# Kernel optimization log

Hardware: AMD Instinct MI355X
Metric: run time of the kernel (lower is better)

## Reference

```python
import jax, jax.numpy as jnp
import numpy as np

D_MODEL = 1024
H = 16
D_K = D_MODEL // H
D_FF = 4096
EPS = 1e-6


def setup_inputs() -> dict:
    key = jax.random.key(0)
    ks = jax.random.split(key, 16)
    s = 1.0 / np.sqrt(D_MODEL)
    sf = 1.0 / np.sqrt(D_FF)
    inp = {
        'x': jax.random.normal(ks[0], (4, 2048, D_MODEL), dtype=jnp.float32),
        'wq': jax.random.uniform(ks[1], (D_MODEL, D_MODEL), minval=-s, maxval=s),
        'bq': jax.random.uniform(ks[2], (D_MODEL,), minval=-s, maxval=s),
        'wk': jax.random.uniform(ks[3], (D_MODEL, D_MODEL), minval=-s, maxval=s),
        'bk': jax.random.uniform(ks[4], (D_MODEL,), minval=-s, maxval=s),
        'wv': jax.random.uniform(ks[5], (D_MODEL, D_MODEL), minval=-s, maxval=s),
        'bv': jax.random.uniform(ks[6], (D_MODEL,), minval=-s, maxval=s),
        'wo': jax.random.uniform(ks[7], (D_MODEL, D_MODEL), minval=-s, maxval=s),
        'bo': jax.random.uniform(ks[8], (D_MODEL,), minval=-s, maxval=s),
        'w1': jax.random.uniform(ks[9], (D_MODEL, D_FF), minval=-s, maxval=s),
        'b1': jax.random.uniform(ks[10], (D_FF,), minval=-s, maxval=s),
        'w2': jax.random.uniform(ks[11], (D_FF, D_MODEL), minval=-sf, maxval=sf),
        'b2': jax.random.uniform(ks[12], (D_MODEL,), minval=-sf, maxval=sf),
        'alpha1': jnp.ones((1,), jnp.float32),
        'bias1': jnp.zeros((1,), jnp.float32),
        'alpha2': jnp.ones((1,), jnp.float32),
        'bias2': jnp.zeros((1,), jnp.float32),
    }
    return inp


def _layer_norm(x, alpha, bias):
    # torch: alpha*(x-mean)/(std+eps)+bias with unbiased std (ddof=1), eps on std
    m = jnp.mean(x, axis=-1, keepdims=True)
    s = jnp.std(x, axis=-1, keepdims=True, ddof=1)
    return alpha * (x - m) / (s + EPS) + bias


def _mha(x, wq, bq, wk, bk, wv, bv, wo, bo):
    B, S, _ = x.shape
    q = (x @ wq + bq).reshape(B, S, H, D_K).transpose(0, 2, 1, 3)
    k = (x @ wk + bk).reshape(B, S, H, D_K).transpose(0, 2, 1, 3)
    v = (x @ wv + bv).reshape(B, S, H, D_K).transpose(0, 2, 1, 3)
    scores = jnp.einsum('bhqd,bhkd->bhqk', q, k) / np.sqrt(D_K)
    attn = jax.nn.softmax(scores, axis=-1)
    out = jnp.einsum('bhqk,bhkd->bhqd', attn, v)
    out = out.transpose(0, 2, 1, 3).reshape(B, S, D_MODEL)
    return out @ wo + bo


def reference(x, wq, bq, wk, bk, wv, bv, wo, bo, w1, b1, w2, b2,
              alpha1, bias1, alpha2, bias2):
    # Residual 1: x + MHA(LN(x))
    h = x + _mha(_layer_norm(x, alpha1, bias1), wq, bq, wk, bk, wv, bv, wo, bo)
    # Residual 2: h + FFN(LN(h)); FFN = W2 relu(W1 z + b1) + b2
    z = _layer_norm(h, alpha2, bias2)
    ffn = jax.nn.relu(z @ w1 + b1) @ w2 + b2
    return h + ffn
```

## Files before the change

### kernel.cpp

```cpp
#include <hip/hip_runtime.h>
#include <hip/hip_bf16.h>
#include <cstdint>
#include <cstddef>

typedef __bf16 bf16;
typedef __bf16 bf16x4 __attribute__((ext_vector_type(4)));
typedef __bf16 bf16x8 __attribute__((ext_vector_type(8)));
typedef float f32x4 __attribute__((ext_vector_type(4)));

#define AS1 __attribute__((address_space(1)))
#define AS3 __attribute__((address_space(3)))

__device__ __forceinline__ void gload_lds16(const void* g, void* l) {
  __builtin_amdgcn_global_load_lds((AS1 void*)g, (AS3 void*)l, 16, 0, 0);
}

__global__ __launch_bounds__(256)
void transpose_cvt(const float* __restrict__ in, bf16* __restrict__ out,
                   int K, int N) {
  __shared__ float t[32][33];
  const int tx = threadIdx.x, ty = threadIdx.y;
  const int n0 = blockIdx.x * 32, k0 = blockIdx.y * 32;
#pragma unroll
  for (int j = ty; j < 32; j += 8)
    t[j][tx] = in[(size_t)(k0 + j) * N + n0 + tx];
  __syncthreads();
#pragma unroll
  for (int j = ty; j < 32; j += 8)
    out[(size_t)(n0 + j) * K + k0 + tx] = (bf16)t[tx][j];
}

__global__ __launch_bounds__(256)
void concat_bias(const float* __restrict__ bq, const float* __restrict__ bk,
                 const float* __restrict__ bv, float* __restrict__ o) {
  int i = blockIdx.x * 256 + threadIdx.x;
  if (i < 1024) o[i] = bq[i];
  else if (i < 2048) o[i] = bk[i - 1024];
  else o[i] = bv[i - 2048];
}

__global__ __launch_bounds__(256)
void ln_kernel(const float* __restrict__ x, bf16* __restrict__ y,
               const float* __restrict__ alpha_p, const float* __restrict__ beta_p) {
  const int row = blockIdx.x;
  const float4 v = ((const float4*)(x + (size_t)row * 1024))[threadIdx.x];
  float s = v.x + v.y + v.z + v.w;
  float ss = v.x * v.x + v.y * v.y + v.z * v.z + v.w * v.w;
#pragma unroll
  for (int m = 1; m < 64; m <<= 1) {
    s += __shfl_xor(s, m);
    ss += __shfl_xor(ss, m);
  }
  __shared__ float red[8];
  const int wave = threadIdx.x >> 6, lane = threadIdx.x & 63;
  if (lane == 0) { red[wave] = s; red[4 + wave] = ss; }
  __syncthreads();
  s = red[0] + red[1] + red[2] + red[3];
  ss = red[4] + red[5] + red[6] + red[7];
  const float mean = s * (1.0f / 1024.0f);
  const float var = fmaxf(ss - 1024.0f * mean * mean, 0.0f) * (1.0f / 1023.0f);
  const float k = alpha_p[0] / (sqrtf(var) + 1e-6f);
  const float beta = beta_p[0];
  union { bf16 b[4]; uint2 u; } pk;
  pk.b[0] = (bf16)((v.x - mean) * k + beta);
  pk.b[1] = (bf16)((v.y - mean) * k + beta);
  pk.b[2] = (bf16)((v.z - mean) * k + beta);
  pk.b[3] = (bf16)((v.w - mean) * k + beta);
  ((uint2*)(y + (size_t)row * 1024))[threadIdx.x] = pk.u;
}

template <typename OutT, bool RELU, bool RESID>
__global__ __launch_bounds__(256)
void gemm_bt(const bf16* __restrict__ A, const bf16* __restrict__ Bt,
             const float* __restrict__ bias, const float* __restrict__ resid,
             OutT* __restrict__ C, int M, int N, int K) {
  __shared__ __align__(16) bf16 As[2][128 * 32];
  __shared__ __align__(16) bf16 Bs[2][128 * 32];
  const int tid = threadIdx.x;
  const int wave = tid >> 6, lane = tid & 63;
  const int l16 = lane & 15, lq = lane >> 4;
  const int nwg = gridDim.x * gridDim.y;
  const int id = blockIdx.y * gridDim.x + blockIdx.x;
  const int w = (id & 7) * (nwg >> 3) + (id >> 3);
  const int bm = (w / gridDim.y) * 128, bn = (w % gridDim.y) * 128;
  const int wr = wave >> 1, wc = wave & 1;

  const int tmp = (lane * 16) ^ (((lane >> 3) & 7) << 4);
  const int srow = tmp >> 6, sseg = (tmp >> 4) & 3;
  const bf16* Ab = A + (size_t)bm * K + sseg * 8;
  const bf16* Bb = Bt + (size_t)bn * K + sseg * 8;

  auto STAGE = [&](int k0, int buf) {
#pragma unroll
    for (int i = 0; i < 2; i++) {
      const int chunk = wave * 2 + i;
      const int r = chunk * 16 + srow;
      gload_lds16(Ab + (size_t)r * K + k0, (char*)As[buf] + chunk * 1024);
      gload_lds16(Bb + (size_t)r * K + k0, (char*)Bs[buf] + chunk * 1024);
    }
  };
  auto swz = [&](int row) -> int {
    return (row >> 1) * 128 + (((((row & 1) << 2) | lq) ^ ((row >> 1) & 7)) << 4);
  };

  STAGE(0, 0);
  __syncthreads();

  f32x4 acc[4][4] = {};
  const int nk = K >> 5;
  for (int t = 0; t < nk; t++) {
    const int cur = t & 1;
    if (t + 1 < nk) STAGE((t + 1) << 5, cur ^ 1);
    bf16x8 a[4], b[4];
#pragma unroll
    for (int m = 0; m < 4; m++)
      a[m] = *(const bf16x8*)((const char*)As[cur] + swz(wr * 64 + m * 16 + l16));
#pragma unroll
    for (int n = 0; n < 4; n++)
      b[n] = *(const bf16x8*)((const char*)Bs[cur] + swz(wc * 64 + n * 16 + l16));
#pragma unroll
    for (int m = 0; m < 4; m++)
#pragma unroll
      for (int n = 0; n < 4; n++)
        acc[m][n] = __builtin_amdgcn_mfma_f32_16x16x32_bf16(a[m], b[n], acc[m][n], 0, 0, 0);
    __syncthreads();
  }
#pragma unroll
  for (int m = 0; m < 4; m++) {
    const int row0 = bm + wr * 64 + m * 16 + lq * 4;
#pragma unroll
    for (int n = 0; n < 4; n++) {
      const int col = bn + wc * 64 + n * 16 + l16;
      const float bv = bias[col];
#pragma unroll
      for (int j = 0; j < 4; j++) {
        float v = acc[m][n][j] + bv;
        if (RELU) v = fmaxf(v, 0.0f);
        if (RESID) v += resid[(size_t)(row0 + j) * N + col];
        C[(size_t)(row0 + j) * N + col] = (OutT)v;
      }
    }
  }
}

__global__ __launch_bounds__(256)
void vt_prep(const bf16* __restrict__ qkv, bf16* __restrict__ Vt) {
  __shared__ __align__(16) bf16 Vl[64 * 64];
  const int tid = threadIdx.x;
  const int sblk = blockIdx.x, bh = blockIdx.y, b = bh >> 4, h = bh & 15;
  const size_t srow = (size_t)b * 2048 + sblk * 64;
  const bf16* src = qkv + srow * 3072 + 2048 + h * 64;
#pragma unroll
  for (int i = 0; i < 2; i++) {
    int c = i * 256 + tid;
    int s = c >> 3, dseg = c & 7;
    int col = dseg ^ (s & 7) ^ (s >> 3);
    *(uint4*)((char*)Vl + s * 128 + col * 16) =
        *(const uint4*)(src + (size_t)s * 3072 + dseg * 8);
  }
  __syncthreads();
  bf16* dst = Vt + (size_t)bh * 64 * 2048 + sblk * 64;
#pragma unroll
  for (int i = 0; i < 2; i++) {
    int c = i * 256 + tid;
    int d = c >> 3, grp = c & 7;
    union { bf16 v[8]; uint4 u; } pk;
#pragma unroll
    for (int j = 0; j < 8; j++) {
      int s = grp * 8 + j;
      int col = (d >> 3) ^ (s & 7) ^ (s >> 3);
      pk.v[j] = *(const bf16*)((char*)Vl + s * 128 + col * 16 + ((2 * d) & 15));
    }
    *(uint4*)(dst + (size_t)d * 2048 + grp * 8) = pk.u;
  }
}

__global__ __launch_bounds__(256, 2)
void attn_kernel(const bf16* __restrict__ qkv, const bf16* __restrict__ Vt,
                 bf16* __restrict__ out) {
  __shared__ __align__(16) bf16 smem[32768];
  bf16* Qs = smem;
  bf16* Ks = smem + 16384;
  bf16* Vs = smem + 24576;
  const int tid = threadIdx.x, wave = tid >> 6, lane = tid & 63;
  const int l16 = lane & 15, lq = lane >> 4;
  const int id = blockIdx.y * 8 + blockIdx.x;
  const int w = (id & 7) * 64 + (id >> 3);
  const int qblk = w & 7, bh = w >> 3;
  const int b = bh >> 4, h = bh & 15;
  const int q0 = qblk * 256;
  const size_t rowbase = (size_t)b * 2048;
  const bf16* Qg = qkv + (rowbase + q0) * 3072 + h * 64;
  const bf16* Kg = qkv + rowbase * 3072 + 1024 + h * 64;
  const bf16* Vg = Vt + (size_t)bh * 64 * 2048;

#pragma unroll
  for (int i = 0; i < 8; i++) {
    const int c = i * 256 + wave * 64;
    const int cl = c + lane;
    const int r = cl >> 3, seg = cl & 7;
    gload_lds16(Qg + (size_t)r * 3072 + (seg ^ (r & 7)) * 8, (char*)Qs + c * 16);
  }
  auto stageKV = [&](int kt, int buf) {
    const int kv0 = kt * 64;
#pragma unroll
    for (int i = 0; i < 2; i++) {
      const int c = i * 256 + wave * 64;
      const int cl = c + lane;
      const int r = cl >> 3, seg = cl & 7;
      gload_lds16(Kg + (size_t)(kv0 + r) * 3072 + (seg ^ (r & 7)) * 8,
                  (char*)Ks + buf * 8192 + c * 16);
      gload_lds16(Vg + (size_t)r * 2048 + kv0 + (seg ^ (r & 7)) * 8,
                  (char*)Vs + buf * 8192 + c * 16);
    }
  };
  stageKV(0, 0);

  f32x4 oacc[4][4] = {};
  f32x4 lacc[4] = {};
  bf16x8 qb[4][2];
  bf16x8 onesb;
#pragma unroll
  for (int j = 0; j < 8; j++) onesb[j] = (bf16)1.0f;

  for (int t = 0; t < 32; t++) {
    const int cur = t & 1;
    __builtin_amdgcn_s_barrier();
    if (t < 31) stageKV(t + 1, cur ^ 1);
    if (t < 31) asm volatile("s_waitcnt vmcnt(4)" ::: "memory");
    else        asm volatile("s_waitcnt vmcnt(0)" ::: "memory");
    __builtin_amdgcn_s_barrier();
    const char* Kb = (const char*)Ks + cur * 8192;
    const char* Vb = (const char*)Vs + cur * 8192;

    if (t == 0) {
#pragma unroll
      for (int g = 0; g < 4; g++)
#pragma unroll
        for (int H = 0; H < 2; H++) {
          const int row = wave * 64 + g * 16 + l16;
          const int col = (H * 64 + lq * 16) ^ ((row & 7) << 4);
          qb[g][H] = *(const bf16x8*)((const char*)Qs + row * 128 + col);
        }
    }
    bf16x8 ka[2][4];
#pragma unroll
    for (int H = 0; H < 2; H++)
#pragma unroll
      for (int m = 0; m < 4; m++) {
        const int row = m * 16 + l16;
        const int col = (H * 64 + lq * 16) ^ ((row & 7) << 4);
        ka[H][m] = *(const bf16x8*)(Kb + row * 128 + col);
      }
    bf16x8 vb[2][4];
#pragma unroll
    for (int H = 0; H < 2; H++)
#pragma unroll
      for (int nd = 0; nd < 4; nd++) {
        const int row = nd * 16 + l16;
        const int xorv = (row & 7) << 4;
        const int c1 = (H * 64 + lq * 8) ^ xorv;
        const int c2 = (H * 64 + lq * 8 + 32) ^ xorv;
        bf16x4 lo = *(const bf16x4*)(Vb + row * 128 + c1);
        bf16x4 hi = *(const bf16x4*)(Vb + row * 128 + c2);
        vb[H][nd] = __builtin_shufflevector(lo, hi, 0, 1, 2, 3, 4, 5, 6, 7);
      }
#pragma unroll
    for (int g = 0; g < 4; g++) {
      f32x4 sc[4];
#pragma unroll
      for (int m = 0; m < 4; m++) {
        f32x4 z = {};
        sc[m] = __builtin_amdgcn_mfma_f32_16x16x32_bf16(ka[0][m], qb[g][0], z, 0, 0, 0);
        sc[m] = __builtin_amdgcn_mfma_f32_16x16x32_bf16(ka[1][m], qb[g][1], sc[m], 0, 0, 0);
      }
      bf16x8 pa0, pa1;
#pragma unroll
      for (int m = 0; m < 2; m++)
#pragma unroll
        for (int r = 0; r < 4; r++)
          pa0[m * 4 + r] = (bf16)__builtin_amdgcn_exp2f(sc[m][r] * 0.1803368801f);
#pragma unroll
      for (int m = 0; m < 2; m++)
#pragma unroll
        for (int r = 0; r < 4; r++)
          pa1[m * 4 + r] = (bf16)__builtin_amdgcn_exp2f(sc[2 + m][r] * 0.1803368801f);
#pragma unroll
      for (int nd = 0; nd < 4; nd++) {
        oacc[g][nd] = __builtin_amdgcn_mfma_f32_16x16x32_bf16(pa0, vb[0][nd], oacc[g][nd], 0, 0, 0);
        oacc[g][nd] = __builtin_amdgcn_mfma_f32_16x16x32_bf16(pa1, vb[1][nd], oacc[g][nd], 0, 0, 0);
      }
      lacc[g] = __builtin_amdgcn_mfma_f32_16x16x32_bf16(pa0, onesb, lacc[g], 0, 0, 0);
      lacc[g] = __builtin_amdgcn_mfma_f32_16x16x32_bf16(pa1, onesb, lacc[g], 0, 0, 0);
    }
  }
#pragma unroll
  for (int g = 0; g < 4; g++) {
#pragma unroll
    for (int r = 0; r < 4; r++) {
      const float inv = 1.0f / lacc[g][r];
      const size_t row = rowbase + q0 + wave * 64 + g * 16 + lq * 4 + r;
#pragma unroll
      for (int nd = 0; nd < 4; nd++)
        out[row * 1024 + h * 64 + nd * 16 + l16] = (bf16)(oacc[g][nd][r] * inv);
    }
  }
}

extern "C" void kernel_launch(void* const* d_in, const int* in_sizes, int n_in,
                              void* d_out, int out_size, void* d_ws, size_t ws_size,
                              hipStream_t stream) {
  const float* x      = (const float*)d_in[0];
  const float* wq     = (const float*)d_in[1];
  const float* bq     = (const float*)d_in[2];
  const float* wk     = (const float*)d_in[3];
  const float* bk     = (const float*)d_in[4];
  const float* wv     = (const float*)d_in[5];
  const float* bv     = (const float*)d_in[6];
  const float* wo     = (const float*)d_in[7];
  const float* bo     = (const float*)d_in[8];
  const float* w1     = (const float*)d_in[9];
  const float* b1     = (const float*)d_in[10];
  const float* w2     = (const float*)d_in[11];
  const float* b2     = (const float*)d_in[12];
  const float* alpha1 = (const float*)d_in[13];
  const float* bias1  = (const float*)d_in[14];
  const float* alpha2 = (const float*)d_in[15];
  const float* bias2  = (const float*)d_in[16];
  float* out = (float*)d_out;

  const size_t MB = 1024ull * 1024ull;
  char* ws = (char*)d_ws;
  bf16*  wqkvT = (bf16*)(ws);
  bf16*  woT   = (bf16*)(ws + 6 * MB);
  bf16*  w1T   = (bf16*)(ws + 8 * MB);
  bf16*  w2T   = (bf16*)(ws + 16 * MB);
  float* bqkv  = (float*)(ws + 24 * MB);
  bf16*  Z     = (bf16*)(ws + 24 * MB + 65536);
  bf16*  Vtb   = Z;
  bf16*  QKV   = (bf16*)(ws + 40 * MB + 65536);
  bf16*  AO    = (bf16*)(ws + 88 * MB + 65536);
  bf16*  FFN1  = QKV;

  const dim3 tb(32, 8);
  transpose_cvt<<<dim3(32, 32), tb, 0, stream>>>(wq, wqkvT, 1024, 1024);
  transpose_cvt<<<dim3(32, 32), tb, 0, stream>>>(wk, wqkvT + 1024 * 1024, 1024, 1024);
  transpose_cvt<<<dim3(32, 32), tb, 0, stream>>>(wv, wqkvT + 2 * 1024 * 1024, 1024, 1024);
  transpose_cvt<<<dim3(32, 32), tb, 0, stream>>>(wo, woT, 1024, 1024);
  transpose_cvt<<<dim3(128, 32), tb, 0, stream>>>(w1, w1T, 1024, 4096);
  transpose_cvt<<<dim3(32, 128), tb, 0, stream>>>(w2, w2T, 4096, 1024);
  concat_bias<<<12, 256, 0, stream>>>(bq, bk, bv, bqkv);

  ln_kernel<<<8192, 256, 0, stream>>>(x, Z, alpha1, bias1);
  gemm_bt<bf16, false, false><<<dim3(64, 24), 256, 0, stream>>>(
      Z, wqkvT, bqkv, nullptr, QKV, 8192, 3072, 1024);
  vt_prep<<<dim3(32, 64), 256, 0, stream>>>(QKV, Vtb);
  attn_kernel<<<dim3(8, 64), 256, 0, stream>>>(QKV, Vtb, AO);
  gemm_bt<float, false, true><<<dim3(64, 8), 256, 0, stream>>>(
      AO, woT, bo, x, out, 8192, 1024, 1024);
  ln_kernel<<<8192, 256, 0, stream>>>(out, Z, alpha2, bias2);
  gemm_bt<bf16, true, false><<<dim3(64, 32), 256, 0, stream>>>(
      Z, w1T, b1, nullptr, FFN1, 8192, 4096, 1024);
  gemm_bt<float, false, true><<<dim3(64, 8), 256, 0, stream>>>(
      FFN1, w2T, b2, out, out, 8192, 1024, 4096);
}
```

Baseline: 381.4 us.

## Add 256x256 triple-buffered GEMM kernel and split-K FFN2 with reduce pass

Adds a new 512-thread GEMM with 256x256 tiles, three-stage LDS buffering via direct global-to-LDS loads, XCD-aware block remapping and split phases interleaving loads with MFMA. It is used for the QKV and FFN1 GEMMs. FFN2 becomes a split-K-by-2 GEMM writing bf16 partials into reused workspace, followed by a reduce kernel that adds the partials, bias and residual. The aim is more data reuse per tile and better occupancy on the long-K FFN2. The cost is extra partial traffic, a bf16 rounding of the partials and an overwrite of the weight workspace.

```diff
diff --git a/kernel.cpp b/kernel.cpp
--- a/kernel.cpp
+++ b/kernel.cpp
@@ -13,6 +13,10 @@
 
 __device__ __forceinline__ void gload_lds16(const void* g, void* l) {
   __builtin_amdgcn_global_load_lds((AS1 void*)g, (AS3 void*)l, 16, 0, 0);
+}
+
+__device__ __forceinline__ float b2f(unsigned short u) {
+  union { unsigned int i; float f; } v; v.i = (unsigned int)u << 16; return v.f;
 }
 
 __global__ __launch_bounds__(256)
@@ -141,6 +145,120 @@
       }
     }
   }
+}
+
+template <typename OutT, bool RELU, bool BIAS>
+__global__ __launch_bounds__(512, 2)
+void gemm_v4(const bf16* __restrict__ A, const bf16* __restrict__ Bt,
+             const float* __restrict__ bias, OutT* __restrict__ C,
+             int lda, int ldb, int ldc, int K,
+             int azs, int bzs, size_t czs) {
+  __shared__ __align__(16) char lds[3 * 32768];
+  const int tid = threadIdx.x;
+  const int wave = tid >> 6, lane = tid & 63;
+  const int l16 = lane & 15, lq = lane >> 4;
+  const int wr = wave >> 2, wc = wave & 3;
+  const int nwg = gridDim.x * gridDim.y;
+  const int id = blockIdx.y * gridDim.x + blockIdx.x;
+  const int w = (id & 7) * (nwg >> 3) + (id >> 3);
+  const int bm = (w / gridDim.y) * 256, bn = (w % gridDim.y) * 256;
+
+  A  += (size_t)blockIdx.z * azs;
+  Bt += (size_t)blockIdx.z * bzs;
+  C  += (size_t)blockIdx.z * czs;
+
+  const int p = lane >> 3, jj = (lane & 7) ^ p;
+  const int lrow = p * 2 + (jj >> 2), lseg = jj & 3;
+  const bf16* Abase = A + (size_t)bm * lda + lseg * 8;
+  const bf16* Bbase = Bt + (size_t)bn * ldb + lseg * 8;
+
+  auto STAGEQ = [&](int t, int qq) {
+    const int k0 = t << 5;
+    const int grow = (qq & 1) * 128 + wave * 16 + lrow;
+    const void* src = (qq < 2) ? (const void*)(Abase + (size_t)grow * lda + k0)
+                               : (const void*)(Bbase + (size_t)grow * ldb + k0);
+    gload_lds16(src, lds + (t % 3) * 32768 + qq * 8192 + wave * 1024);
+  };
+  auto swz = [&](int row) -> int {
+    return (row >> 1) * 128 + (((((row & 1) << 2) | lq) ^ ((row >> 1) & 7)) << 4);
+  };
+
+  const int nk = K >> 5;
+#pragma unroll
+  for (int qq = 0; qq < 4; qq++) STAGEQ(0, qq);
+#pragma unroll
+  for (int qq = 0; qq < 4; qq++) STAGEQ(1, qq);
+
+  f32x4 acc[8][4] = {};
+  for (int t = 0; t < nk; t++) {
+    const char* buf = lds + (t % 3) * 32768;
+    if (t + 1 < nk) asm volatile("s_waitcnt vmcnt(4)" ::: "memory");
+    else            asm volatile("s_waitcnt vmcnt(0)" ::: "memory");
+    __builtin_amdgcn_s_barrier();
+    if (t + 2 < nk) { STAGEQ(t + 2, 0); STAGEQ(t + 2, 1); }
+    bf16x8 a0[4], b0[4];
+#pragma unroll
+    for (int i = 0; i < 4; i++)
+      a0[i] = *(const bf16x8*)(buf + swz(wr * 128 + i * 16 + l16));
+#pragma unroll
+    for (int n = 0; n < 4; n++)
+      b0[n] = *(const bf16x8*)(buf + 16384 + swz(wc * 64 + n * 16 + l16));
+    __builtin_amdgcn_s_barrier();
+    asm volatile("s_waitcnt lgkmcnt(0)" ::: "memory");
+    __builtin_amdgcn_sched_barrier(0);
+    __builtin_amdgcn_s_setprio(1);
+#pragma unroll
+    for (int i = 0; i < 4; i++)
+#pragma unroll
+      for (int n = 0; n < 4; n++)
+        acc[i][n] = __builtin_amdgcn_mfma_f32_16x16x32_bf16(a0[i], b0[n], acc[i][n], 0, 0, 0);
+    __builtin_amdgcn_s_setprio(0);
+    if (t + 2 < nk) { STAGEQ(t + 2, 2); STAGEQ(t + 2, 3); }
+    bf16x8 a1[4];
+#pragma unroll
+    for (int i = 0; i < 4; i++)
+      a1[i] = *(const bf16x8*)(buf + swz(wr * 128 + 64 + i * 16 + l16));
+    __builtin_amdgcn_s_barrier();
+    asm volatile("s_waitcnt lgkmcnt(0)" ::: "memory");
+    __builtin_amdgcn_sched_barrier(0);
+    __builtin_amdgcn_s_setprio(1);
+#pragma unroll
+    for (int i = 0; i < 4; i++)
+#pragma unroll
+      for (int n = 0; n < 4; n++)
+        acc[4 + i][n] = __builtin_amdgcn_mfma_f32_16x16x32_bf16(a1[i], b0[n], acc[4 + i][n], 0, 0, 0);
+    __builtin_amdgcn_s_setprio(0);
+  }
+#pragma unroll
+  for (int m = 0; m < 8; m++) {
+    const int row0 = bm + wr * 128 + m * 16 + lq * 4;
+#pragma unroll
+    for (int n = 0; n < 4; n++) {
+      const int col = bn + wc * 64 + n * 16 + l16;
+      const float bv = BIAS ? bias[col] : 0.0f;
+#pragma unroll
+      for (int j = 0; j < 4; j++) {
+        float v = acc[m][n][j] + bv;
+        if (RELU) v = fmaxf(v, 0.0f);
+        C[(size_t)(row0 + j) * ldc + col] = (OutT)v;
+      }
+    }
+  }
+}
+
+__global__ __launch_bounds__(256)
+void ffn2_reduce(const bf16* __restrict__ p0, const bf16* __restrict__ p1,
+                 const float* __restrict__ b2, float* __restrict__ out) {
+  const size_t i = (size_t)blockIdx.x * 256 + threadIdx.x;
+  float4 h = ((const float4*)out)[i];
+  const ushort4 a = ((const ushort4*)p0)[i];
+  const ushort4 b = ((const ushort4*)p1)[i];
+  const float4 bb = ((const float4*)b2)[i & 255];
+  h.x += b2f(a.x) + b2f(b.x) + bb.x;
+  h.y += b2f(a.y) + b2f(b.y) + bb.y;
+  h.z += b2f(a.z) + b2f(b.z) + bb.z;
+  h.w += b2f(a.w) + b2f(b.w) + bb.w;
+  ((float4*)out)[i] = h;
 }
 
 __global__ __launch_bounds__(256)
@@ -341,6 +459,8 @@
   bf16*  QKV   = (bf16*)(ws + 40 * MB + 65536);
   bf16*  AO    = (bf16*)(ws + 88 * MB + 65536);
   bf16*  FFN1  = QKV;
+  bf16*  PART  = (bf16*)ws;
+  const size_t PART1_OFF = (24 * MB + 65536) / 2;
 
   const dim3 tb(32, 8);
   transpose_cvt<<<dim3(32, 32), tb, 0, stream>>>(wq, wqkvT, 1024, 1024);
@@ -352,15 +472,16 @@
   concat_bias<<<12, 256, 0, stream>>>(bq, bk, bv, bqkv);
 
   ln_kernel<<<8192, 256, 0, stream>>>(x, Z, alpha1, bias1);
-  gemm_bt<bf16, false, false><<<dim3(64, 24), 256, 0, stream>>>(
-      Z, wqkvT, bqkv, nullptr, QKV, 8192, 3072, 1024);
+  gemm_v4<bf16, false, true><<<dim3(32, 12), 512, 0, stream>>>(
+      Z, wqkvT, bqkv, QKV, 1024, 1024, 3072, 1024, 0, 0, 0);
   vt_prep<<<dim3(32, 64), 256, 0, stream>>>(QKV, Vtb);
   attn_kernel<<<dim3(8, 64), 256, 0, stream>>>(QKV, Vtb, AO);
   gemm_bt<float, false, true><<<dim3(64, 8), 256, 0, stream>>>(
       AO, woT, bo, x, out, 8192, 1024, 1024);
   ln_kernel<<<8192, 256, 0, stream>>>(out, Z, alpha2, bias2);
-  gemm_bt<bf16, true, false><<<dim3(64, 32), 256, 0, stream>>>(
-      Z, w1T, b1, nullptr, FFN1, 8192, 4096, 1024);
-  gemm_bt<float, false, true><<<dim3(64, 8), 256, 0, stream>>>(
-      FFN1, w2T, b2, out, out, 8192, 1024, 4096);
-}
+  gemm_v4<bf16, true, true><<<dim3(32, 16), 512, 0, stream>>>(
+      Z, w1T, b1, FFN1, 1024, 1024, 4096, 1024, 0, 0, 0);
+  gemm_v4<bf16, false, false><<<dim3(32, 4, 2), 512, 0, stream>>>(
+      FFN1, w2T, nullptr, PART, 4096, 4096, 1024, 2048, 2048, 2048, PART1_OFF);
+  ffn2_reduce<<<8192, 256, 0, stream>>>(PART, PART + PART1_OFF, b2, out);
+}
```

Result: faster. 373.0 us (-2.2%).
